# Kernel optimization log

Hardware: AMD Instinct MI355X
Metric: run time of the kernel (lower is better)

Reference implementation:

```python
import jax, jax.numpy as jnp
import numpy as np

B, S, H = 1, 1024, 2048
E, F, FS = 32, 768, 4096
TOP_K = 4
SCALE = 0.02


def setup_inputs() -> dict:
    key = jax.random.key(0)
    ks = jax.random.split(key, 9)
    return {
        "hidden_states": jax.random.normal(ks[0], (B, S, H), jnp.float32),
        "router_weight": jax.random.normal(ks[1], (E, H), jnp.float32) * SCALE,
        "w_gate": jax.random.normal(ks[2], (E, H, F), jnp.float32) * SCALE,
        "w_up": jax.random.normal(ks[3], (E, H, F), jnp.float32) * SCALE,
        "w_down": jax.random.normal(ks[4], (E, F, H), jnp.float32) * SCALE,
        "sw_gate": jax.random.normal(ks[5], (H, FS), jnp.float32) * SCALE,
        "sw_up": jax.random.normal(ks[6], (H, FS), jnp.float32) * SCALE,
        "sw_down": jax.random.normal(ks[7], (FS, H), jnp.float32) * SCALE,
        "sgate_w": jax.random.normal(ks[8], (H, 1), jnp.float32) * SCALE,
    }


def reference(hidden_states, router_weight, w_gate, w_up, w_down,
              sw_gate, sw_up, sw_down, sgate_w):
    b, s, h = hidden_states.shape
    x = hidden_states.reshape(-1, h)                      # [T,H]
    T = x.shape[0]

    # ---- router: linear -> softmax (fp32) -> topk -> renormalize ----
    logits = x @ router_weight.T                          # [T,E]
    probs = jax.nn.softmax(logits.astype(jnp.float32), axis=-1)
    topv, topi = jax.lax.top_k(probs, TOP_K)              # [T,K]
    topv = topv / jnp.sum(topv, axis=-1, keepdims=True)
    topv = topv.astype(probs.dtype)

    # combine weights: scatter topk weights into dense [T,E] mask
    combine = jnp.zeros((T, E), probs.dtype).at[
        jnp.arange(T)[:, None], topi].add(topv)

    # ---- experts: SwiGLU per expert, weighted combine ----
    g = jnp.einsum('th,ehf->etf', x, w_gate)              # [E,T,F]
    u = jnp.einsum('th,ehf->etf', x, w_up)                # [E,T,F]
    act = jax.nn.silu(g) * u                              # [E,T,F]
    out = jnp.einsum('te,etf,efh->th', combine, act, w_down)  # [T,H]

    # ---- shared expert with sigmoid gate ----
    shared = (jax.nn.silu(x @ sw_gate) * (x @ sw_up)) @ sw_down  # [T,H]
    out = out + jax.nn.sigmoid(x @ sgate_w) * shared

    return out.reshape(b, s, h)
```

## Files before the change

kernel.cpp:

```cpp
#include <hip/hip_runtime.h>
#include <math.h>

#define T_TOK 1024
#define H_DIM 2048
#define N_EXP 32
#define TOPK  4
#define F_DIM 768
#define FS_DIM 4096
#define FS_HALF 2048

typedef __bf16 bf16;
typedef __attribute__((ext_vector_type(4))) __bf16 bf16x4;
typedef __attribute__((ext_vector_type(8))) __bf16 bf16x8;
typedef __attribute__((ext_vector_type(4))) float f32x4;

#define BAR() do {                                        \
    asm volatile("s_waitcnt lgkmcnt(0)" ::: "memory");    \
    __builtin_amdgcn_s_barrier();                         \
    __builtin_amdgcn_sched_barrier(0);                    \
  } while (0)

__device__ __forceinline__ int swz(int row, int colB) {
  return row * 64 + (colB ^ (((row >> 2) & 3) << 4));
}

__global__ __launch_bounds__(256) void router_kernel(
    const float* __restrict__ x, const float* __restrict__ rw,
    const float* __restrict__ sgw,
    float* __restrict__ topw, float* __restrict__ sg,
    int* __restrict__ counts, int* __restrict__ lists)
{
  int t = blockIdx.x; int tid = threadIdx.x;
  int lane = tid & 63, wave = tid >> 6;
  float acc[N_EXP];
  #pragma unroll
  for (int e = 0; e < N_EXP; e++) acc[e] = 0.f;
  float accs = 0.f;
  const float* xr = x + (size_t)t * H_DIM;
  for (int h = tid; h < H_DIM; h += 256) {
    float xv = xr[h];
    accs += xv * sgw[h];
    #pragma unroll
    for (int e = 0; e < N_EXP; e++) acc[e] += xv * rw[e * H_DIM + h];
  }
  __shared__ float red[4][N_EXP];
  __shared__ float reds[4];
  __shared__ float logits[N_EXP];
  #pragma unroll
  for (int e = 0; e < N_EXP; e++) {
    float v = acc[e];
    for (int off = 32; off; off >>= 1) v += __shfl_down(v, off, 64);
    if (lane == 0) red[wave][e] = v;
  }
  {
    float v = accs;
    for (int off = 32; off; off >>= 1) v += __shfl_down(v, off, 64);
    if (lane == 0) reds[wave] = v;
  }
  __syncthreads();
  if (tid < N_EXP) logits[tid] = red[0][tid] + red[1][tid] + red[2][tid] + red[3][tid];
  __syncthreads();
  if (tid == 0) {
    float m = -1e30f;
    #pragma unroll
    for (int e = 0; e < N_EXP; e++) m = fmaxf(m, logits[e]);
    float p[N_EXP];
    #pragma unroll
    for (int e = 0; e < N_EXP; e++) p[e] = expf(logits[e] - m);
    int ids[TOPK]; float vs[TOPK]; float wsum = 0.f;
    #pragma unroll
    for (int k = 0; k < TOPK; k++) {
      int best = 0; float bv = -1.f;
      for (int e = 0; e < N_EXP; e++) {
        if (p[e] > bv) { bv = p[e]; best = e; }
      }
      ids[k] = best; vs[k] = bv; wsum += bv; p[best] = -2.f;
    }
    float inv = 1.f / wsum;
    float sgs = reds[0] + reds[1] + reds[2] + reds[3];
    sg[t] = 1.f / (1.f + expf(-sgs));
    #pragma unroll
    for (int k = 0; k < TOPK; k++) {
      int slot = t * TOPK + k;
      topw[slot] = vs[k] * inv;
      int pos = atomicAdd(&counts[ids[k]], 1);
      lists[ids[k] * T_TOK + pos] = slot;
    }
  }
}

__global__ __launch_bounds__(512) __attribute__((amdgpu_waves_per_eu(4, 4)))
void gateup_fused(
    const float* __restrict__ X,
    const float* __restrict__ wg_, const float* __restrict__ wu_,
    const float* __restrict__ swg, const float* __restrict__ swu,
    bf16* __restrict__ act, bf16* __restrict__ acts,
    const int* __restrict__ lists, const int* __restrict__ counts,
    int n_shared, int sh_nfb, int actsN, int col_off)
{
  int id = blockIdx.x;
  bool gather = id >= n_shared;
  const float *Wg, *Wu; const int* lb = nullptr;
  int count, mt, fb, ldb, Nout; bf16* C;
  if (gather) {
    int g = id - n_shared;
    int j = g >> 3;
    int e = (g & 7) + 8 * (j / 96);
    int rr = j % 96;
    mt = (rr / 6) * 64; fb = (rr % 6) * 128;
    count = counts[e]; lb = lists + e * T_TOK;
    Wg = wg_ + (size_t)e * H_DIM * F_DIM;
    Wu = wu_ + (size_t)e * H_DIM * F_DIM;
    ldb = F_DIM; Nout = F_DIM; C = act;
  } else {
    fb = (id % sh_nfb) * 128; mt = (id / sh_nfb) * 64;
    count = T_TOK; ldb = FS_DIM; Nout = actsN;
    Wg = swg + col_off; Wu = swu + col_off;
    C = acts;
  }
  if (mt >= count) return;

  __shared__ alignas(16) char sA [2][64 * 64];
  __shared__ alignas(16) char sBg[2][128 * 64];
  __shared__ alignas(16) char sBu[2][128 * 64];

  int tid = threadIdx.x;
  int lane = tid & 63, wid = tid >> 6;
  int wr = wid >> 2, wc = wid & 3;
  int l15 = lane & 15, qB = (lane >> 4) << 4;

  const float* aptr;
  {
    int r = mt + (tid >> 3);
    int rc = r < count ? r : count - 1;
    int tok = gather ? (lb[rc] >> 2) : rc;
    aptr = X + (size_t)tok * H_DIM + ((tid & 7) << 2);
  }
  int t8 = tid & 255;
  int bng = t8 & 31;
  int bk4 = (t8 >> 5) << 2;
  const float* bptr = (tid < 256 ? Wg : Wu) + (size_t)bk4 * ldb + fb + bng * 4;
  char* bds = (tid < 256) ? &sBg[0][0] : &sBu[0][0];

  f32x4 accg[2][2], accu[2][2];
  #pragma unroll
  for (int m = 0; m < 2; m++)
    #pragma unroll
    for (int n = 0; n < 2; n++) {
      accg[m][n] = (f32x4){0.f,0.f,0.f,0.f};
      accu[m][n] = (f32x4){0.f,0.f,0.f,0.f};
    }

  f32x4 ava, bva[4];
  f32x4 avb, bvb[4];

  #define GU_ISSUE(av, bv, k0) do {                                   \
    av = *(const f32x4*)(aptr + (k0));                                \
    _Pragma("unroll")                                                 \
    for (int r_ = 0; r_ < 4; r_++)                                    \
      bv[r_] = *(const f32x4*)(bptr + (size_t)((k0) + r_) * ldb);     \
    __builtin_amdgcn_sched_barrier(0);                                \
  } while (0)

  #define GU_STAGE(b, av, bv) do {                                    \
    bf16x4 ta;                                                        \
    ta[0]=(bf16)av[0]; ta[1]=(bf16)av[1];                             \
    ta[2]=(bf16)av[2]; ta[3]=(bf16)av[3];                             \
    *(bf16x4*)(sA[b] + swz(tid >> 3, (tid & 7) << 3)) = ta;           \
    _Pragma("unroll")                                                 \
    for (int i_ = 0; i_ < 4; i_++) {                                  \
      bf16x4 tb;                                                      \
      tb[0]=(bf16)bv[0][i_]; tb[1]=(bf16)bv[1][i_];                   \
      tb[2]=(bf16)bv[2][i_]; tb[3]=(bf16)bv[3][i_];                   \
      *(bf16x4*)(bds + (b) * (128 * 64) + swz(bng * 4 + i_, bk4 << 1)) = tb; \
    } } while (0)

  #define GU_MFMA(b) do {                                             \
    __builtin_amdgcn_s_setprio(1);                                    \
    bf16x8 af0 = *(const bf16x8*)(sA[b] + swz(wr * 32 + l15, qB));    \
    bf16x8 af1 = *(const bf16x8*)(sA[b] + swz(wr * 32 + 16 + l15, qB)); \
    _Pragma("unroll")                                                 \
    for (int n_ = 0; n_ < 2; n_++) {                                  \
      int rb = wc * 32 + n_ * 16 + l15;                               \
      bf16x8 bg = *(const bf16x8*)(sBg[b] + swz(rb, qB));             \
      bf16x8 bu = *(const bf16x8*)(sBu[b] + swz(rb, qB));             \
      accg[0][n_] = __builtin_amdgcn_mfma_f32_16x16x32_bf16(af0, bg, accg[0][n_], 0,0,0); \
      accg[1][n_] = __builtin_amdgcn_mfma_f32_16x16x32_bf16(af1, bg, accg[1][n_], 0,0,0); \
      accu[0][n_] = __builtin_amdgcn_mfma_f32_16x16x32_bf16(af0, bu, accu[0][n_], 0,0,0); \
      accu[1][n_] = __builtin_amdgcn_mfma_f32_16x16x32_bf16(af1, bu, accu[1][n_], 0,0,0); \
    }                                                                 \
    __builtin_amdgcn_s_setprio(0);                                    \
  } while (0)

  const int NT = H_DIM / 32;
  GU_ISSUE(ava, bva, 0);
  GU_ISSUE(avb, bvb, 32);
  GU_STAGE(0, ava, bva);
  GU_ISSUE(ava, bva, 64);
  BAR();
  for (int t = 0; t < NT; t += 2) {
    GU_MFMA(0);
    GU_STAGE(1, avb, bvb);
    if (t + 3 < NT) GU_ISSUE(avb, bvb, (t + 3) * 32);
    BAR();
    GU_MFMA(1);
    if (t + 2 < NT) {
      GU_STAGE(0, ava, bva);
      if (t + 4 < NT) GU_ISSUE(ava, bva, (t + 4) * 32);
    }
    BAR();
  }
  #undef GU_ISSUE
  #undef GU_STAGE
  #undef GU_MFMA

  #pragma unroll
  for (int m = 0; m < 2; m++) {
    #pragma unroll
    for (int q = 0; q < 4; q++) {
      int gr = mt + wr * 32 + m * 16 + (lane >> 4) * 4 + q;
      if (gr < count) {
        size_t rowo = (gather ? (size_t)lb[gr] : (size_t)gr) * Nout;
        #pragma unroll
        for (int n = 0; n < 2; n++) {
          float g = accg[m][n][q], u = accu[m][n][q];
          C[rowo + fb + wc * 32 + n * 16 + l15] =
              (bf16)(g / (1.f + __expf(-g)) * u);
        }
      }
    }
  }
}

__global__ __launch_bounds__(256, 4) void down_fused(
    const bf16* __restrict__ act, const bf16* __restrict__ acts,
    const float* __restrict__ wd_, const float* __restrict__ swd,
    bf16* __restrict__ dslot, float* __restrict__ out,
    const float* __restrict__ sg,
    const int* __restrict__ lists, const int* __restrict__ counts,
    int n_shared, int lda_sh, int kd_sh, int swd_off, int accum)
{
  int id = blockIdx.x;
  bool expert = id >= n_shared;
  const bf16* A; const float* W; const int* lb = nullptr;
  int count, mt, nb, Kd, lda;
  if (expert) {
    int g = id - n_shared;
    int j = g >> 3;
    int e = (g & 7) + 8 * (j >> 7);
    int rr = j & 127;
    nb = (rr & 15) * 128; mt = (rr >> 4) * 64;
    count = counts[e]; lb = lists + e * T_TOK;
    A = act; lda = F_DIM; Kd = F_DIM;
    W = wd_ + (size_t)e * F_DIM * H_DIM;
  } else {
    nb = (id & 15) * 128; mt = (id >> 4) * 64;
    count = T_TOK; A = acts; lda = lda_sh; Kd = kd_sh;
    W = swd + (size_t)swd_off * H_DIM;
  }
  if (mt >= count) return;

  __shared__ alignas(16) char sA[2][64 * 64];
  __shared__ alignas(16) char sB[2][128 * 64];

  int tid = threadIdx.x;
  int lane = tid & 63, wid = tid >> 6;
  int wr = wid >> 1, wc = wid & 1;
  int l15 = lane & 15, qB = (lane >> 4) << 4;
  int bng = tid & 31;
  int bk4 = (tid >> 5) << 2;

  const bf16* aptr;
  {
    int r = mt + (tid >> 2);
    int rc = r < count ? r : count - 1;
    int ar = expert ? lb[rc] : rc;
    aptr = A + (size_t)ar * lda + ((tid & 3) << 3);
  }
  const float* bptr = W + (size_t)bk4 * H_DIM + nb + bng * 4;

  f32x4 acc[2][4];
  #pragma unroll
  for (int m = 0; m < 2; m++)
    #pragma unroll
    for (int n = 0; n < 4; n++)
      acc[m][n] = (f32x4){0.f,0.f,0.f,0.f};

  uint4 ava, avb; f32x4 bva[4], bvb[4];

  #define DN_ISSUE(av, bv, k0) do {                                   \
    av = *(const uint4*)(aptr + (k0));                                \
    _Pragma("unroll")                                                 \
    for (int r_ = 0; r_ < 4; r_++)                                    \
      bv[r_] = *(const f32x4*)(bptr + (size_t)((k0) + r_) * H_DIM);   \
    } while (0)

  #define DN_STAGE(b, av, bv) do {                                    \
    *(uint4*)(sA[b] + swz(tid >> 2, (tid & 3) << 4)) = av;            \
    _Pragma("unroll")                                                 \
    for (int i_ = 0; i_ < 4; i_++) {                                  \
      bf16x4 tb;                                                      \
      tb[0]=(bf16)bv[0][i_]; tb[1]=(bf16)bv[1][i_];                   \
      tb[2]=(bf16)bv[2][i_]; tb[3]=(bf16)bv[3][i_];                   \
      *(bf16x4*)(sB[b] + swz(bng * 4 + i_, bk4 << 1)) = tb;           \
    } } while (0)

  #define DN_MFMA(b) do {                                             \
    __builtin_amdgcn_s_setprio(1);                                    \
    bf16x8 af0 = *(const bf16x8*)(sA[b] + swz(wr * 32 + l15, qB));    \
    bf16x8 af1 = *(const bf16x8*)(sA[b] + swz(wr * 32 + 16 + l15, qB)); \
    _Pragma("unroll")                                                 \
    for (int n_ = 0; n_ < 4; n_++) {                                  \
      bf16x8 bb = *(const bf16x8*)(sB[b] + swz(wc * 64 + n_ * 16 + l15, qB)); \
      acc[0][n_] = __builtin_amdgcn_mfma_f32_16x16x32_bf16(af0, bb, acc[0][n_], 0,0,0); \
      acc[1][n_] = __builtin_amdgcn_mfma_f32_16x16x32_bf16(af1, bb, acc[1][n_], 0,0,0); \
    }                                                                 \
    __builtin_amdgcn_s_setprio(0);                                    \
  } while (0)

  const int NT = Kd / 32;
  DN_ISSUE(ava, bva, 0);
  DN_ISSUE(avb, bvb, 32);
  DN_STAGE(0, ava, bva);
  DN_ISSUE(ava, bva, 64);
  BAR();
  for (int t = 0; t < NT; t += 2) {
    DN_MFMA(0);
    DN_STAGE(1, avb, bvb);
    if (t + 3 < NT) DN_ISSUE(avb, bvb, (t + 3) * 32);
    BAR();
    DN_MFMA(1);
    if (t + 2 < NT) {
      DN_STAGE(0, ava, bva);
      if (t + 4 < NT) DN_ISSUE(ava, bva, (t + 4) * 32);
    }
    BAR();
  }
  #undef DN_ISSUE
  #undef DN_STAGE
  #undef DN_MFMA

  #pragma unroll
  for (int m = 0; m < 2; m++) {
    #pragma unroll
    for (int q = 0; q < 4; q++) {
      int gr = mt + wr * 32 + m * 16 + (lane >> 4) * 4 + q;
      if (gr < count) {
        #pragma unroll
        for (int n = 0; n < 4; n++) {
          int col = nb + wc * 64 + n * 16 + l15;
          if (expert) {
            dslot[(size_t)lb[gr] * H_DIM + col] = (bf16)acc[m][n][q];
          } else if (!accum) {
            out[(size_t)gr * H_DIM + col] = sg[gr] * acc[m][n][q];
          } else {
            out[(size_t)gr * H_DIM + col] += sg[gr] * acc[m][n][q];
          }
        }
      }
    }
  }
}

__global__ __launch_bounds__(256) void combine_kernel(
    const bf16* __restrict__ dslot, const float* __restrict__ topw,
    float* __restrict__ out)
{
  int t = blockIdx.x;
  int h = threadIdx.x * 8;
  float w0 = topw[t * 4 + 0], w1 = topw[t * 4 + 1];
  float w2 = topw[t * 4 + 2], w3 = topw[t * 4 + 3];
  bf16x8 a0 = *(const bf16x8*)&dslot[(size_t)(t * 4 + 0) * H_DIM + h];
  bf16x8 a1 = *(const bf16x8*)&dslot[(size_t)(t * 4 + 1) * H_DIM + h];
  bf16x8 a2 = *(const bf16x8*)&dslot[(size_t)(t * 4 + 2) * H_DIM + h];
  bf16x8 a3 = *(const bf16x8*)&dslot[(size_t)(t * 4 + 3) * H_DIM + h];
  f32x4 o0 = *(f32x4*)&out[(size_t)t * H_DIM + h];
  f32x4 o1 = *(f32x4*)&out[(size_t)t * H_DIM + h + 4];
  float o[8] = {o0[0], o0[1], o0[2], o0[3], o1[0], o1[1], o1[2], o1[3]};
  #pragma unroll
  for (int j = 0; j < 8; j++)
    o[j] += w0 * (float)a0[j] + w1 * (float)a1[j] + w2 * (float)a2[j]
          + w3 * (float)a3[j];
  *(f32x4*)&out[(size_t)t * H_DIM + h]     = (f32x4){o[0], o[1], o[2], o[3]};
  *(f32x4*)&out[(size_t)t * H_DIM + h + 4] = (f32x4){o[4], o[5], o[6], o[7]};
}

extern "C" void kernel_launch(void* const* d_in, const int* in_sizes, int n_in,
                              void* d_out, int out_size, void* d_ws, size_t ws_size,
                              hipStream_t stream) {
  const float* x   = (const float*)d_in[0];
  const float* rw  = (const float*)d_in[1];
  const float* wg  = (const float*)d_in[2];
  const float* wu  = (const float*)d_in[3];
  const float* wd  = (const float*)d_in[4];
  const float* swg = (const float*)d_in[5];
  const float* swu = (const float*)d_in[6];
  const float* swd = (const float*)d_in[7];
  const float* sgw = (const float*)d_in[8];
  float* out = (float*)d_out;
  char* ws = (char*)d_ws;

  bool fullfs = ws_size >= (size_t)32000000;
  size_t actsN = fullfs ? FS_DIM : FS_HALF;
  int sh_nfb = (int)(actsN / 128);
  int nsh_gu = sh_nfb * (T_TOK / 64);

  size_t off = 0;
  int*   counts  = (int*)(ws + off); off += 256;
  int*   lists   = (int*)(ws + off); off += (size_t)N_EXP * T_TOK * 4;
  float* topw    = (float*)(ws + off); off += (size_t)T_TOK * TOPK * 4;
  float* sg      = (float*)(ws + off); off += (size_t)T_TOK * 4;
  bf16*  act     = (bf16*)(ws + off); off += (size_t)T_TOK * TOPK * F_DIM * 2;
  bf16*  acts    = (bf16*)(ws + off); off += (size_t)T_TOK * actsN * 2;
  bf16*  dslot   = (bf16*)(ws + off); off += (size_t)T_TOK * TOPK * H_DIM * 2;

  hipMemsetAsync(counts, 0, 256, stream);

  router_kernel<<<T_TOK, 256, 0, stream>>>(x, rw, sgw, topw, sg, counts, lists);

  const int EXP_GU = N_EXP * 96;
  const int DN_EXP = N_EXP * 128;

  if (fullfs) {
    gateup_fused<<<nsh_gu + EXP_GU, 512, 0, stream>>>(
        x, wg, wu, swg, swu, act, acts, lists, counts,
        nsh_gu, sh_nfb, FS_DIM, 0);
    down_fused<<<256 + DN_EXP, 256, 0, stream>>>(
        act, acts, wd, swd, dslot, out, sg, lists, counts,
        256, FS_DIM, FS_DIM, 0, 0);
  } else {
    gateup_fused<<<nsh_gu + EXP_GU, 512, 0, stream>>>(
        x, wg, wu, swg, swu, act, acts, lists, counts,
        nsh_gu, sh_nfb, FS_HALF, 0);
    down_fused<<<256 + DN_EXP, 256, 0, stream>>>(
        act, acts, wd, swd, dslot, out, sg, lists, counts,
        256, FS_HALF, FS_HALF, 0, 0);
    gateup_fused<<<nsh_gu, 512, 0, stream>>>(
        x, wg, wu, swg, swu, act, acts, lists, counts,
        nsh_gu, sh_nfb, FS_HALF, FS_HALF);
    down_fused<<<256, 256, 0, stream>>>(
        act, acts, wd, swd, dslot, out, sg, lists, counts,
        256, FS_HALF, FS_HALF, FS_HALF, 1);
  }
  combine_kernel<<<T_TOK, 256, 0, stream>>>(dslot, topw, out);
}
```

Before: 375.4 us.

## Pre-convert activations to bf16 and split down projection into shared and half-width expert passes

Adds a kernel that converts x to bf16 once, so gate/up blocks load half the A bytes and skip per-tile conversion. The fused down kernel is split into separate shared and expert kernels. The expert down projection and combine now run in two column halves with a half-size slot buffer, which shrinks the workspace and removes the full-FS path. The cost is more kernel launches and always taking the two-pass shared path even when the workspace would fit the full width.

```diff
diff --git a/kernel.cpp b/kernel.cpp
--- a/kernel.cpp
+++ b/kernel.cpp
@@ -8,6 +8,7 @@
 #define F_DIM 768
 #define FS_DIM 4096
 #define FS_HALF 2048
+#define H_HALF 1024
 
 typedef __bf16 bf16;
 typedef __attribute__((ext_vector_type(4))) __bf16 bf16x4;
@@ -89,9 +90,21 @@
   }
 }
 
+__global__ __launch_bounds__(256) void xcvt_kernel(
+    const float* __restrict__ x, bf16* __restrict__ xb)
+{
+  size_t i = ((size_t)blockIdx.x * 256 + threadIdx.x) * 8;
+  f32x4 a = *(const f32x4*)(x + i);
+  f32x4 b = *(const f32x4*)(x + i + 4);
+  bf16x8 o;
+  #pragma unroll
+  for (int j = 0; j < 4; j++) { o[j] = (bf16)a[j]; o[4 + j] = (bf16)b[j]; }
+  *(bf16x8*)(xb + i) = o;
+}
+
 __global__ __launch_bounds__(512) __attribute__((amdgpu_waves_per_eu(4, 4)))
 void gateup_fused(
-    const float* __restrict__ X,
+    const bf16* __restrict__ XB,
     const float* __restrict__ wg_, const float* __restrict__ wu_,
     const float* __restrict__ swg, const float* __restrict__ swu,
     bf16* __restrict__ act, bf16* __restrict__ acts,
@@ -129,12 +142,12 @@
   int wr = wid >> 2, wc = wid & 3;
   int l15 = lane & 15, qB = (lane >> 4) << 4;
 
-  const float* aptr;
+  const bf16* aptr;
   {
     int r = mt + (tid >> 3);
     int rc = r < count ? r : count - 1;
     int tok = gather ? (lb[rc] >> 2) : rc;
-    aptr = X + (size_t)tok * H_DIM + ((tid & 7) << 2);
+    aptr = XB + (size_t)tok * H_DIM + ((tid & 7) << 2);
   }
   int t8 = tid & 255;
   int bng = t8 & 31;
@@ -151,11 +164,10 @@
       accu[m][n] = (f32x4){0.f,0.f,0.f,0.f};
     }
 
-  f32x4 ava, bva[4];
-  f32x4 avb, bvb[4];
+  uint2 ava, avb; f32x4 bva[4], bvb[4];
 
   #define GU_ISSUE(av, bv, k0) do {                                   \
-    av = *(const f32x4*)(aptr + (k0));                                \
+    av = *(const uint2*)(aptr + (k0));                                \
     _Pragma("unroll")                                                 \
     for (int r_ = 0; r_ < 4; r_++)                                    \
       bv[r_] = *(const f32x4*)(bptr + (size_t)((k0) + r_) * ldb);     \
@@ -163,10 +175,7 @@
   } while (0)
 
   #define GU_STAGE(b, av, bv) do {                                    \
-    bf16x4 ta;                                                        \
-    ta[0]=(bf16)av[0]; ta[1]=(bf16)av[1];                             \
-    ta[2]=(bf16)av[2]; ta[3]=(bf16)av[3];                             \
-    *(bf16x4*)(sA[b] + swz(tid >> 3, (tid & 7) << 3)) = ta;           \
+    *(uint2*)(sA[b] + swz(tid >> 3, (tid & 7) << 3)) = av;            \
     _Pragma("unroll")                                                 \
     for (int i_ = 0; i_ < 4; i_++) {                                  \
       bf16x4 tb;                                                      \
@@ -232,33 +241,15 @@
   }
 }
 
-__global__ __launch_bounds__(256, 4) void down_fused(
-    const bf16* __restrict__ act, const bf16* __restrict__ acts,
-    const float* __restrict__ wd_, const float* __restrict__ swd,
-    bf16* __restrict__ dslot, float* __restrict__ out,
-    const float* __restrict__ sg,
-    const int* __restrict__ lists, const int* __restrict__ counts,
-    int n_shared, int lda_sh, int kd_sh, int swd_off, int accum)
+__global__ __launch_bounds__(256, 4) void dn_shared(
+    const bf16* __restrict__ acts, const float* __restrict__ swd,
+    float* __restrict__ out, const float* __restrict__ sg,
+    int lda_sh, int kd_sh, int swd_off, int accum)
 {
   int id = blockIdx.x;
-  bool expert = id >= n_shared;
-  const bf16* A; const float* W; const int* lb = nullptr;
-  int count, mt, nb, Kd, lda;
-  if (expert) {
-    int g = id - n_shared;
-    int j = g >> 3;
-    int e = (g & 7) + 8 * (j >> 7);
-    int rr = j & 127;
-    nb = (rr & 15) * 128; mt = (rr >> 4) * 64;
-    count = counts[e]; lb = lists + e * T_TOK;
-    A = act; lda = F_DIM; Kd = F_DIM;
-    W = wd_ + (size_t)e * F_DIM * H_DIM;
-  } else {
-    nb = (id & 15) * 128; mt = (id >> 4) * 64;
-    count = T_TOK; A = acts; lda = lda_sh; Kd = kd_sh;
-    W = swd + (size_t)swd_off * H_DIM;
-  }
-  if (mt >= count) return;
+  int nb = (id & 15) * 128, mt = (id >> 4) * 64;
+  const bf16* A = acts; int lda = lda_sh, Kd = kd_sh;
+  const float* W = swd + (size_t)swd_off * H_DIM;
 
   __shared__ alignas(16) char sA[2][64 * 64];
   __shared__ alignas(16) char sB[2][128 * 64];
@@ -270,13 +261,7 @@
   int bng = tid & 31;
   int bk4 = (tid >> 5) << 2;
 
-  const bf16* aptr;
-  {
-    int r = mt + (tid >> 2);
-    int rc = r < count ? r : count - 1;
-    int ar = expert ? lb[rc] : rc;
-    aptr = A + (size_t)ar * lda + ((tid & 3) << 3);
-  }
+  const bf16* aptr = A + (size_t)(mt + (tid >> 2)) * lda + ((tid & 3) << 3);
   const float* bptr = W + (size_t)bk4 * H_DIM + nb + bng * 4;
 
   f32x4 acc[2][4];
@@ -345,44 +330,146 @@
     #pragma unroll
     for (int q = 0; q < 4; q++) {
       int gr = mt + wr * 32 + m * 16 + (lane >> 4) * 4 + q;
+      #pragma unroll
+      for (int n = 0; n < 4; n++) {
+        int col = nb + wc * 64 + n * 16 + l15;
+        if (!accum) out[(size_t)gr * H_DIM + col] = sg[gr] * acc[m][n][q];
+        else        out[(size_t)gr * H_DIM + col] += sg[gr] * acc[m][n][q];
+      }
+    }
+  }
+}
+
+__global__ __launch_bounds__(256, 4) void dn_expert(
+    const bf16* __restrict__ act, const float* __restrict__ wd_,
+    bf16* __restrict__ dsloth,
+    const int* __restrict__ lists, const int* __restrict__ counts,
+    int colbase)
+{
+  int g = blockIdx.x;
+  int j = g >> 3;
+  int e = (g & 7) + 8 * (j >> 7);
+  int rr = j & 127;
+  int nbl = (rr & 7) * 128;
+  int mt = (rr >> 3) * 64;
+  int count = counts[e];
+  const int* lb = lists + e * T_TOK;
+  if (mt >= count) return;
+  const float* W = wd_ + (size_t)e * F_DIM * H_DIM;
+
+  __shared__ alignas(16) char sA[2][64 * 64];
+  __shared__ alignas(16) char sB[2][128 * 64];
+
+  int tid = threadIdx.x;
+  int lane = tid & 63, wid = tid >> 6;
+  int wr = wid >> 1, wc = wid & 1;
+  int l15 = lane & 15, qB = (lane >> 4) << 4;
+  int bng = tid & 31;
+  int bk4 = (tid >> 5) << 2;
+
+  const bf16* aptr;
+  {
+    int r = mt + (tid >> 2);
+    int rc = r < count ? r : count - 1;
+    aptr = act + (size_t)lb[rc] * F_DIM + ((tid & 3) << 3);
+  }
+  const float* bptr = W + (size_t)bk4 * H_DIM + colbase + nbl + bng * 4;
+
+  f32x4 acc[2][4];
+  #pragma unroll
+  for (int m = 0; m < 2; m++)
+    #pragma unroll
+    for (int n = 0; n < 4; n++)
+      acc[m][n] = (f32x4){0.f,0.f,0.f,0.f};
+
+  uint4 ava, avb; f32x4 bva[4], bvb[4];
+
+  #define DE_ISSUE(av, bv, k0) do {                                   \
+    av = *(const uint4*)(aptr + (k0));                                \
+    _Pragma("unroll")                                                 \
+    for (int r_ = 0; r_ < 4; r_++)                                    \
+      bv[r_] = *(const f32x4*)(bptr + (size_t)((k0) + r_) * H_DIM);   \
+    } while (0)
+
+  #define DE_STAGE(b, av, bv) do {                                    \
+    *(uint4*)(sA[b] + swz(tid >> 2, (tid & 3) << 4)) = av;            \
+    _Pragma("unroll")                                                 \
+    for (int i_ = 0; i_ < 4; i_++) {                                  \
+      bf16x4 tb;                                                      \
+      tb[0]=(bf16)bv[0][i_]; tb[1]=(bf16)bv[1][i_];                   \
+      tb[2]=(bf16)bv[2][i_]; tb[3]=(bf16)bv[3][i_];                   \
+      *(bf16x4*)(sB[b] + swz(bng * 4 + i_, bk4 << 1)) = tb;           \
+    } } while (0)
+
+  #define DE_MFMA(b) do {                                             \
+    __builtin_amdgcn_s_setprio(1);                                    \
+    bf16x8 af0 = *(const bf16x8*)(sA[b] + swz(wr * 32 + l15, qB));    \
+    bf16x8 af1 = *(const bf16x8*)(sA[b] + swz(wr * 32 + 16 + l15, qB)); \
+    _Pragma("unroll")                                                 \
+    for (int n_ = 0; n_ < 4; n_++) {                                  \
+      bf16x8 bb = *(const bf16x8*)(sB[b] + swz(wc * 64 + n_ * 16 + l15, qB)); \
+      acc[0][n_] = __builtin_amdgcn_mfma_f32_16x16x32_bf16(af0, bb, acc[0][n_], 0,0,0); \
+      acc[1][n_] = __builtin_amdgcn_mfma_f32_16x16x32_bf16(af1, bb, acc[1][n_], 0,0,0); \
+    }                                                                 \
+    __builtin_amdgcn_s_setprio(0);                                    \
+  } while (0)
+
+  const int NT = F_DIM / 32;
+  DE_ISSUE(ava, bva, 0);
+  DE_ISSUE(avb, bvb, 32);
+  DE_STAGE(0, ava, bva);
+  DE_ISSUE(ava, bva, 64);
+  BAR();
+  for (int t = 0; t < NT; t += 2) {
+    DE_MFMA(0);
+    DE_STAGE(1, avb, bvb);
+    if (t + 3 < NT) DE_ISSUE(avb, bvb, (t + 3) * 32);
+    BAR();
+    DE_MFMA(1);
+    if (t + 2 < NT) {
+      DE_STAGE(0, ava, bva);
+      if (t + 4 < NT) DE_ISSUE(ava, bva, (t + 4) * 32);
+    }
+    BAR();
+  }
+  #undef DE_ISSUE
+  #undef DE_STAGE
+  #undef DE_MFMA
+
+  #pragma unroll
+  for (int m = 0; m < 2; m++) {
+    #pragma unroll
+    for (int q = 0; q < 4; q++) {
+      int gr = mt + wr * 32 + m * 16 + (lane >> 4) * 4 + q;
       if (gr < count) {
         #pragma unroll
         for (int n = 0; n < 4; n++) {
-          int col = nb + wc * 64 + n * 16 + l15;
-          if (expert) {
-            dslot[(size_t)lb[gr] * H_DIM + col] = (bf16)acc[m][n][q];
-          } else if (!accum) {
-            out[(size_t)gr * H_DIM + col] = sg[gr] * acc[m][n][q];
-          } else {
-            out[(size_t)gr * H_DIM + col] += sg[gr] * acc[m][n][q];
-          }
+          int col = nbl + wc * 64 + n * 16 + l15;
+          dsloth[(size_t)lb[gr] * H_HALF + col] = (bf16)acc[m][n][q];
         }
       }
     }
   }
 }
 
-__global__ __launch_bounds__(256) void combine_kernel(
-    const bf16* __restrict__ dslot, const float* __restrict__ topw,
-    float* __restrict__ out)
+__global__ __launch_bounds__(256) void combine_half(
+    const bf16* __restrict__ dsloth, const float* __restrict__ topw,
+    float* __restrict__ out, int colbase)
 {
   int t = blockIdx.x;
-  int h = threadIdx.x * 8;
+  int c = threadIdx.x * 4;
   float w0 = topw[t * 4 + 0], w1 = topw[t * 4 + 1];
   float w2 = topw[t * 4 + 2], w3 = topw[t * 4 + 3];
-  bf16x8 a0 = *(const bf16x8*)&dslot[(size_t)(t * 4 + 0) * H_DIM + h];
-  bf16x8 a1 = *(const bf16x8*)&dslot[(size_t)(t * 4 + 1) * H_DIM + h];
-  bf16x8 a2 = *(const bf16x8*)&dslot[(size_t)(t * 4 + 2) * H_DIM + h];
-  bf16x8 a3 = *(const bf16x8*)&dslot[(size_t)(t * 4 + 3) * H_DIM + h];
-  f32x4 o0 = *(f32x4*)&out[(size_t)t * H_DIM + h];
-  f32x4 o1 = *(f32x4*)&out[(size_t)t * H_DIM + h + 4];
-  float o[8] = {o0[0], o0[1], o0[2], o0[3], o1[0], o1[1], o1[2], o1[3]};
-  #pragma unroll
-  for (int j = 0; j < 8; j++)
+  bf16x4 a0 = *(const bf16x4*)&dsloth[(size_t)(t * 4 + 0) * H_HALF + c];
+  bf16x4 a1 = *(const bf16x4*)&dsloth[(size_t)(t * 4 + 1) * H_HALF + c];
+  bf16x4 a2 = *(const bf16x4*)&dsloth[(size_t)(t * 4 + 2) * H_HALF + c];
+  bf16x4 a3 = *(const bf16x4*)&dsloth[(size_t)(t * 4 + 3) * H_HALF + c];
+  f32x4 o = *(f32x4*)&out[(size_t)t * H_DIM + colbase + c];
+  #pragma unroll
+  for (int j = 0; j < 4; j++)
     o[j] += w0 * (float)a0[j] + w1 * (float)a1[j] + w2 * (float)a2[j]
           + w3 * (float)a3[j];
-  *(f32x4*)&out[(size_t)t * H_DIM + h]     = (f32x4){o[0], o[1], o[2], o[3]};
-  *(f32x4*)&out[(size_t)t * H_DIM + h + 4] = (f32x4){o[4], o[5], o[6], o[7]};
+  *(f32x4*)&out[(size_t)t * H_DIM + colbase + c] = o;
 }
 
 extern "C" void kernel_launch(void* const* d_in, const int* in_sizes, int n_in,
@@ -400,47 +487,36 @@
   float* out = (float*)d_out;
   char* ws = (char*)d_ws;
 
-  bool fullfs = ws_size >= (size_t)32000000;
-  size_t actsN = fullfs ? FS_DIM : FS_HALF;
-  int sh_nfb = (int)(actsN / 128);
-  int nsh_gu = sh_nfb * (T_TOK / 64);
-
   size_t off = 0;
-  int*   counts  = (int*)(ws + off); off += 256;
-  int*   lists   = (int*)(ws + off); off += (size_t)N_EXP * T_TOK * 4;
-  float* topw    = (float*)(ws + off); off += (size_t)T_TOK * TOPK * 4;
-  float* sg      = (float*)(ws + off); off += (size_t)T_TOK * 4;
-  bf16*  act     = (bf16*)(ws + off); off += (size_t)T_TOK * TOPK * F_DIM * 2;
-  bf16*  acts    = (bf16*)(ws + off); off += (size_t)T_TOK * actsN * 2;
-  bf16*  dslot   = (bf16*)(ws + off); off += (size_t)T_TOK * TOPK * H_DIM * 2;
+  int*   counts = (int*)(ws + off); off += 256;
+  int*   lists  = (int*)(ws + off); off += (size_t)N_EXP * T_TOK * 4;
+  float* topw   = (float*)(ws + off); off += (size_t)T_TOK * TOPK * 4;
+  float* sg     = (float*)(ws + off); off += (size_t)T_TOK * 4;
+  bf16*  xb     = (bf16*)(ws + off); off += (size_t)T_TOK * H_DIM * 2;
+  bf16*  act    = (bf16*)(ws + off); off += (size_t)T_TOK * TOPK * F_DIM * 2;
+  bf16*  acts   = (bf16*)(ws + off); off += (size_t)T_TOK * FS_HALF * 2;
+  bf16*  dsloth = (bf16*)(ws + off); off += (size_t)T_TOK * TOPK * H_HALF * 2;
 
   hipMemsetAsync(counts, 0, 256, stream);
 
   router_kernel<<<T_TOK, 256, 0, stream>>>(x, rw, sgw, topw, sg, counts, lists);
-
+  xcvt_kernel<<<(T_TOK * H_DIM) / 2048, 256, 0, stream>>>(x, xb);
+
+  const int SH_NFB = FS_HALF / 128;
+  const int NSH_GU = SH_NFB * (T_TOK / 64);
   const int EXP_GU = N_EXP * 96;
-  const int DN_EXP = N_EXP * 128;
-
-  if (fullfs) {
-    gateup_fused<<<nsh_gu + EXP_GU, 512, 0, stream>>>(
-        x, wg, wu, swg, swu, act, acts, lists, counts,
-        nsh_gu, sh_nfb, FS_DIM, 0);
-    down_fused<<<256 + DN_EXP, 256, 0, stream>>>(
-        act, acts, wd, swd, dslot, out, sg, lists, counts,
-        256, FS_DIM, FS_DIM, 0, 0);
-  } else {
-    gateup_fused<<<nsh_gu + EXP_GU, 512, 0, stream>>>(
-        x, wg, wu, swg, swu, act, acts, lists, counts,
-        nsh_gu, sh_nfb, FS_HALF, 0);
-    down_fused<<<256 + DN_EXP, 256, 0, stream>>>(
-        act, acts, wd, swd, dslot, out, sg, lists, counts,
-        256, FS_HALF, FS_HALF, 0, 0);
-    gateup_fused<<<nsh_gu, 512, 0, stream>>>(
-        x, wg, wu, swg, swu, act, acts, lists, counts,
-        nsh_gu, sh_nfb, FS_HALF, FS_HALF);
-    down_fused<<<256, 256, 0, stream>>>(
-        act, acts, wd, swd, dslot, out, sg, lists, counts,
-        256, FS_HALF, FS_HALF, FS_HALF, 1);
-  }
-  combine_kernel<<<T_TOK, 256, 0, stream>>>(dslot, topw, out);
-}
+
+  gateup_fused<<<NSH_GU + EXP_GU, 512, 0, stream>>>(
+      xb, wg, wu, swg, swu, act, acts, lists, counts,
+      NSH_GU, SH_NFB, FS_HALF, 0);
+  dn_shared<<<256, 256, 0, stream>>>(acts, swd, out, sg, FS_HALF, FS_HALF, 0, 0);
+  gateup_fused<<<NSH_GU, 512, 0, stream>>>(
+      xb, wg, wu, swg, swu, act, acts, lists, counts,
+      NSH_GU, SH_NFB, FS_HALF, FS_HALF);
+  dn_shared<<<256, 256, 0, stream>>>(acts, swd, out, sg, FS_HALF, FS_HALF, FS_HALF, 1);
+
+  dn_expert<<<N_EXP * 128, 256, 0, stream>>>(act, wd, dsloth, lists, counts, 0);
+  combine_half<<<T_TOK, 256, 0, stream>>>(dsloth, topw, out, 0);
+  dn_expert<<<N_EXP * 128, 256, 0, stream>>>(act, wd, dsloth, lists, counts, H_HALF);
+  combine_half<<<T_TOK, 256, 0, stream>>>(dsloth, topw, out, H_HALF);
+}
```

Result: slower. 438.5 us (+16.8%).
